# Kernel optimization log

Measured on AMD Instinct MI355X. Metric: run time of the kernel, lower is better.

The kernel has to match this reference:

```python
import jax, jax.numpy as jnp
import numpy as np

D_MODEL = 1024
N_HEADS = 16
D_HEAD = D_MODEL // N_HEADS
B, T = 4, 2048


def setup_inputs() -> dict:
    key = jax.random.key(0)
    ks = jax.random.split(key, 9)
    s = 0.02
    return {
        "x": jax.random.normal(ks[0], (B, T, D_MODEL), dtype=jnp.float32),
        "Wq": jax.random.normal(ks[1], (D_MODEL, D_MODEL), dtype=jnp.float32) * s,
        "bq": jnp.zeros((D_MODEL,), dtype=jnp.float32),
        "Wk": jax.random.normal(ks[2], (D_MODEL, D_MODEL), dtype=jnp.float32) * s,
        "bk": jnp.zeros((D_MODEL,), dtype=jnp.float32),
        "Wv": jax.random.normal(ks[3], (D_MODEL, D_MODEL), dtype=jnp.float32) * s,
        "bv": jnp.zeros((D_MODEL,), dtype=jnp.float32),
        "Wo": jax.random.normal(ks[4], (D_MODEL, D_MODEL), dtype=jnp.float32) * s,
        "bo": jnp.zeros((D_MODEL,), dtype=jnp.float32),
    }


def reference(x, Wq, bq, Wk, bk, Wv, bv, Wo, bo):
    # Dropout in eval mode (identity), as standard for a correctness baseline.
    Bx, Tx, _ = x.shape
    # torch nn.Linear: y = x @ W.T + b
    Q = x @ Wq.T + bq
    K = x @ Wk.T + bk
    V = x @ Wv.T + bv
    # [B, T, H, Dh] -> [B, H, T, Dh]
    Q = Q.reshape(Bx, Tx, N_HEADS, D_HEAD).transpose(0, 2, 1, 3)
    K = K.reshape(Bx, Tx, N_HEADS, D_HEAD).transpose(0, 2, 1, 3)
    V = V.reshape(Bx, Tx, N_HEADS, D_HEAD).transpose(0, 2, 1, 3)
    scale = 1.0 / jnp.sqrt(jnp.float32(D_HEAD))
    scores = jnp.einsum("bhqd,bhkd->bhqk", Q, K) * scale  # [B,H,T,T]
    # additive causal mask: -1e6 above the diagonal (matches torch.triu trick)
    mask = jnp.triu(jnp.full((Tx, Tx), -1000000.0, dtype=scores.dtype), k=1)
    scores = scores + mask
    attn = jax.nn.softmax(scores, axis=-1)
    out = jnp.einsum("bhqk,bhkd->bhqd", attn, V)  # [B,H,T,Dh]
    out = out.transpose(0, 2, 1, 3).reshape(Bx, Tx, D_MODEL)
    out = out @ Wo.T + bo
    return out
```

## Files before the change

kernel.cpp:

```cpp
#include <hip/hip_runtime.h>
#include <stdint.h>

#define DM 1024
#define HEADS 16
#define DH 64
#define BQ 4
#define TT 2048
#define MTOT (BQ*TT)
#define NQT (TT/64)

typedef __attribute__((ext_vector_type(8))) __bf16 bf16x8;
typedef __attribute__((ext_vector_type(4))) float f32x4;
typedef __attribute__((ext_vector_type(4))) uint32_t u32x4;
typedef unsigned short u16;
typedef __attribute__((ext_vector_type(8))) unsigned short u16x8;

__device__ __forceinline__ u16 f2b(float f) {
  uint32_t u = __builtin_bit_cast(uint32_t, f);
  u = (u + 0x7fffu + ((u >> 16) & 1u)) >> 16;
  return (u16)u;
}

__device__ __forceinline__ uint32_t cvtpk(float lo, float hi) {
  uint32_t r;
  asm("v_cvt_pk_bf16_f32 %0, %1, %2" : "=v"(r) : "v"(lo), "v"(hi));
  return r;
}

__device__ __forceinline__ void gload_lds16(const u16* g, u16* l) {
  __builtin_amdgcn_global_load_lds(
      (const __attribute__((address_space(1))) void*)g,
      (__attribute__((address_space(3))) void*)l, 16, 0, 0);
}

#define NX (MTOT * DM / 4)
#define NW (DM * DM / 4)
__global__ __launch_bounds__(256) void cast_all(const float* __restrict__ x,
                                                const float* __restrict__ Wq,
                                                const float* __restrict__ Wk,
                                                const float* __restrict__ Wv,
                                                const float* __restrict__ Wo,
                                                u16* __restrict__ xb,
                                                u16* __restrict__ wqkvb,
                                                u16* __restrict__ wob) {
  int i = blockIdx.x * 256 + threadIdx.x;
  const float* src; u16* dst;
  if (i < NX)               { src = x;  dst = xb; }
  else if (i < NX + NW)     { src = Wq; dst = wqkvb;          i -= NX; }
  else if (i < NX + 2 * NW) { src = Wk; dst = wqkvb + 4 * NW; i -= NX + NW; }
  else if (i < NX + 3 * NW) { src = Wv; dst = wqkvb + 8 * NW; i -= NX + 2 * NW; }
  else                      { src = Wo; dst = wob;            i -= NX + 3 * NW; }
  float4 v = ((const float4*)src)[i];
  ushort4 o;
  o.x = f2b(v.x); o.y = f2b(v.y); o.z = f2b(v.z); o.w = f2b(v.w);
  ((ushort4*)dst)[i] = o;
}

#define BKq 32
#define NKq (DM / BKq)
#define SLOT_A (256 * BKq)
#define SLOT_E (2 * SLOT_A)

__global__ __launch_bounds__(512, 2) void gemm_qkv8(const u16* __restrict__ A,
                                                    const u16* __restrict__ W,
                                                    const float* __restrict__ bq,
                                                    const float* __restrict__ bk,
                                                    const float* __restrict__ bv,
                                                    u16* __restrict__ Qo,
                                                    u16* __restrict__ Ko,
                                                    u16* __restrict__ Vto,
                                                    float qs) {
  __shared__ u16 lds[4 * SLOT_E];
  const int tid = threadIdx.x, lane = tid & 63, wave = tid >> 6;
  const int fr = lane & 15, g = lane >> 4;
  const int wm = wave >> 2, wn = wave & 3;

  int bid = blockIdx.x;
  bid = (bid & 7) * 48 + (bid >> 3);
  const int bx = bid % 12, by = bid / 12;
  const int m0 = by * 256, n0 = bx * 256;

  const int srow = tid >> 2;
  const int schunk = (tid & 3) ^ ((tid >> 3) & 3);
  const u16* gA0 = A + (size_t)(m0 + srow) * DM + schunk * 8;
  const u16* gA1 = gA0 + (size_t)128 * DM;
  const u16* gB0 = W + (size_t)(n0 + srow) * DM + schunk * 8;
  const u16* gB1 = gB0 + (size_t)128 * DM;
  const int dA0 = wave * 512;
  const int dA1 = 4096 + wave * 512;
  const int dB0 = SLOT_A + wave * 512;
  const int dB1 = SLOT_A + 4096 + wave * 512;

#define STAGE_Ah(slot, kt) {                                 \
    u16* ls = &lds[(slot) * SLOT_E];                         \
    const int ke = (kt) * BKq;                               \
    gload_lds16(gA0 + ke, ls + dA0);                         \
    gload_lds16(gA1 + ke, ls + dA1); }
#define STAGE_Bh(slot, kt) {                                 \
    u16* ls = &lds[(slot) * SLOT_E];                         \
    const int ke = (kt) * BKq;                               \
    gload_lds16(gB0 + ke, ls + dB0);                         \
    gload_lds16(gB1 + ke, ls + dB1); }

  const int rchunk = (g ^ ((fr >> 1) & 3)) * 8;
  const int offA = (wm * 128 + fr) * 32 + rchunk;
  const int offB = SLOT_A + (wn * 64 + fr) * 32 + rchunk;

  f32x4 acc[8][4];
#pragma unroll
  for (int mi = 0; mi < 8; ++mi)
#pragma unroll
    for (int ni = 0; ni < 4; ++ni) acc[mi][ni] = (f32x4){0.f, 0.f, 0.f, 0.f};

  bf16x8 afA[8], bfA[4], afB[8], bfB[4];

#define READ_P1(AFv, BFv, kt) {                              \
    const u16* sl = &lds[((kt) & 3) * SLOT_E];               \
    _Pragma("unroll")                                        \
    for (int mi = 0; mi < 4; ++mi)                           \
      AFv[mi] = *(const bf16x8*)&sl[offA + mi * 512];        \
    _Pragma("unroll")                                        \
    for (int ni = 0; ni < 4; ++ni)                           \
      BFv[ni] = *(const bf16x8*)&sl[offB + ni * 512]; }
#define READ_P2(AFv, kt) {                                   \
    const u16* sl = &lds[((kt) & 3) * SLOT_E];               \
    _Pragma("unroll")                                        \
    for (int mi = 4; mi < 8; ++mi)                           \
      AFv[mi] = *(const bf16x8*)&sl[offA + mi * 512]; }

#define MFMA_P1(AFv, BFv) {                                  \
    __builtin_amdgcn_s_setprio(1);                           \
    _Pragma("unroll")                                        \
    for (int mi = 0; mi < 4; ++mi)                           \
      _Pragma("unroll")                                      \
      for (int ni = 0; ni < 4; ++ni)                         \
        acc[mi][ni] = __builtin_amdgcn_mfma_f32_16x16x32_bf16(AFv[mi], BFv[ni], acc[mi][ni], 0, 0, 0); \
    __builtin_amdgcn_s_setprio(0); }
#define MFMA_P2(AFv, BFv) {                                  \
    __builtin_amdgcn_s_setprio(1);                           \
    _Pragma("unroll")                                        \
    for (int mi = 4; mi < 8; ++mi)                           \
      _Pragma("unroll")                                      \
      for (int ni = 0; ni < 4; ++ni)                         \
        acc[mi][ni] = __builtin_amdgcn_mfma_f32_16x16x32_bf16(AFv[mi], BFv[ni], acc[mi][ni], 0, 0, 0); \
    __builtin_amdgcn_s_setprio(0); }

#define BARQ asm volatile("s_barrier" ::: "memory");
#define WAIT4 asm volatile("s_waitcnt vmcnt(4)" ::: "memory"); BARQ
#define WAIT0 asm volatile("s_waitcnt vmcnt(0)" ::: "memory"); BARQ

#define STEP(AFc, BFc, AFn, BFn, kt, DO_STAGE) {             \
    WAIT4                                                    \
    READ_P1(AFn, BFn, (kt) + 1)                              \
    MFMA_P1(AFc, BFc)                                        \
    if (DO_STAGE) STAGE_Ah(((kt) + 3) & 3, (kt) + 3)         \
    BARQ                                                     \
    READ_P2(AFn, (kt) + 1)                                   \
    MFMA_P2(AFc, BFc)                                        \
    if (DO_STAGE) STAGE_Bh(((kt) + 3) & 3, (kt) + 3) }

  STAGE_Ah(0, 0) STAGE_Bh(0, 0)
  STAGE_Ah(1, 1) STAGE_Bh(1, 1)
  STAGE_Ah(2, 2) STAGE_Bh(2, 2)
  asm volatile("s_waitcnt vmcnt(8)" ::: "memory");
  asm volatile("s_barrier" ::: "memory");
  READ_P1(afA, bfA, 0)
  READ_P2(afA, 0)

  for (int kt = 0; kt < NKq - 4; kt += 2) {
    STEP(afA, bfA, afB, bfB, kt, true)
    STEP(afB, bfB, afA, bfA, kt + 1, true)
  }
  STEP(afA, bfA, afB, bfB, NKq - 4, true)
  STEP(afB, bfB, afA, bfA, NKq - 3, false)
  WAIT0
  READ_P1(afB, bfB, NKq - 1)
  MFMA_P1(afA, bfA)
  BARQ
  READ_P2(afB, NKq - 1)
  MFMA_P2(afA, bfA)
  MFMA_P1(afB, bfB)
  MFMA_P2(afB, bfB)

  const int g4 = g * 4;
  const int seg = n0 >> 10;
  const int nbase = (n0 & 1023) + wn * 64 + fr;
  if (seg == 0) {
#pragma unroll
    for (int ni = 0; ni < 4; ++ni) {
      const int cgl = nbase + ni * 16;
      const float bb = bq[cgl];
      const int hh = cgl >> 6, d = cgl & 63;
#pragma unroll
      for (int mi = 0; mi < 8; ++mi) {
        const int m = m0 + wm * 128 + mi * 16 + g4;
        const int bi = m >> 11, t = m & 2047;
        u16* dst = &Qo[(((size_t)bi * HEADS + hh) * TT + t) * DH + d];
#pragma unroll
        for (int j = 0; j < 4; ++j)
          dst[(size_t)j * DH] = f2b((acc[mi][ni][j] + bb) * qs);
      }
    }
  } else if (seg == 1) {
#pragma unroll
    for (int ni = 0; ni < 4; ++ni) {
      const int cgl = nbase + ni * 16;
      const float bb = bk[cgl];
      const int hh = cgl >> 6, d = cgl & 63;
#pragma unroll
      for (int mi = 0; mi < 8; ++mi) {
        const int m = m0 + wm * 128 + mi * 16 + g4;
        const int bi = m >> 11, t = m & 2047;
        u16* dst = &Ko[(((size_t)bi * HEADS + hh) * TT + t) * DH + d];
#pragma unroll
        for (int j = 0; j < 4; ++j)
          dst[(size_t)j * DH] = f2b(acc[mi][ni][j] + bb);
      }
    }
  } else {
#pragma unroll
    for (int ni = 0; ni < 4; ++ni) {
      const int cgl = nbase + ni * 16;
      const float bb = bv[cgl];
      const int hh = cgl >> 6, d = cgl & 63;
#pragma unroll
      for (int mi = 0; mi < 8; ++mi) {
        const int t0 = (m0 + wm * 128 + mi * 16 + g4) & 2047;
        const int bi = (m0 + wm * 128 + mi * 16 + g4) >> 11;
        const int w64 = t0 & 63;
        const int pos = (t0 & ~63) | (((w64 >> 5) & 1) << 5) | (((w64 >> 2) & 3) << 3) |
                        (((w64 >> 4) & 1) << 2);
        ushort4 o;
        o.x = f2b(acc[mi][ni][0] + bb);
        o.y = f2b(acc[mi][ni][1] + bb);
        o.z = f2b(acc[mi][ni][2] + bb);
        o.w = f2b(acc[mi][ni][3] + bb);
        *(ushort4*)&Vto[(((size_t)bi * HEADS + hh) * DH + d) * TT + pos] = o;
      }
    }
  }
#undef STAGE_Ah
#undef STAGE_Bh
#undef READ_P1
#undef READ_P2
#undef MFMA_P1
#undef MFMA_P2
#undef STEP
#undef BARQ
#undef WAIT4
#undef WAIT0
}

#define SLOT_OA (256 * 32)
#define SLOT_OB (128 * 32)
#define SLOT_OE (SLOT_OA + SLOT_OB)

__global__ __launch_bounds__(512, 2) void gemm_out8(const u16* __restrict__ A,
                                                    const u16* __restrict__ Bw,
                                                    const float* __restrict__ bias,
                                                    float* __restrict__ outp) {
  __shared__ u16 lds[4 * SLOT_OE];
  const int tid = threadIdx.x, lane = tid & 63, wave = tid >> 6;
  const int fr = lane & 15, g = lane >> 4;
  const int wm = wave >> 1, wn = wave & 1;

  const int bx = blockIdx.x >> 5, by = blockIdx.x & 31;
  const int m0 = by * 256, n0 = bx * 128;

  const int srow = tid >> 2;
  const int schunk = (tid & 3) ^ ((tid >> 3) & 3);
  const u16* gA0 = A + (size_t)(m0 + srow) * DM + schunk * 8;
  const u16* gA1 = gA0 + (size_t)128 * DM;
  const u16* gB0 = Bw + (size_t)(n0 + srow) * DM + schunk * 8;
  const int dA0 = wave * 512;
  const int dA1 = 4096 + wave * 512;
  const int dB0 = SLOT_OA + wave * 512;

#define STAGEO(slot, kt) {                                   \
    u16* ls = &lds[(slot) * SLOT_OE];                        \
    const int ke = (kt) * 32;                                \
    gload_lds16(gA0 + ke, ls + dA0);                         \
    gload_lds16(gA1 + ke, ls + dA1);                         \
    gload_lds16(gB0 + ke, ls + dB0); }

  const int rchunk = (g ^ ((fr >> 1) & 3)) * 8;
  const int offA = (wm * 64 + fr) * 32 + rchunk;
  const int offB = SLOT_OA + (wn * 64 + fr) * 32 + rchunk;

  f32x4 acc[4][4];
#pragma unroll
  for (int mi = 0; mi < 4; ++mi)
#pragma unroll
    for (int ni = 0; ni < 4; ++ni) acc[mi][ni] = (f32x4){0.f, 0.f, 0.f, 0.f};

  bf16x8 afA[4], bfA[4], afB[4], bfB[4];

#define READO(AFv, BFv, kt) {                                \
    const u16* sl = &lds[((kt) & 3) * SLOT_OE];              \
    _Pragma("unroll")                                        \
    for (int mi = 0; mi < 4; ++mi)                           \
      AFv[mi] = *(const bf16x8*)&sl[offA + mi * 512];        \
    _Pragma("unroll")                                        \
    for (int ni = 0; ni < 4; ++ni)                           \
      BFv[ni] = *(const bf16x8*)&sl[offB + ni * 512]; }

#define MFMAO(AFv, BFv) {                                    \
    __builtin_amdgcn_s_setprio(1);                           \
    _Pragma("unroll")                                        \
    for (int mi = 0; mi < 4; ++mi)                           \
      _Pragma("unroll")                                      \
      for (int ni = 0; ni < 4; ++ni)                         \
        acc[mi][ni] = __builtin_amdgcn_mfma_f32_16x16x32_bf16(AFv[mi], BFv[ni], acc[mi][ni], 0, 0, 0); \
    __builtin_amdgcn_s_setprio(0); }

#define OW3 asm volatile("s_waitcnt vmcnt(3)" ::: "memory"); \
            asm volatile("s_barrier" ::: "memory");
#define OW0 asm volatile("s_waitcnt vmcnt(0)" ::: "memory"); \
            asm volatile("s_barrier" ::: "memory");

  STAGEO(0, 0)
  STAGEO(1, 1)
  STAGEO(2, 2)
  asm volatile("s_waitcnt vmcnt(6)" ::: "memory");
  asm volatile("s_barrier" ::: "memory");
  READO(afA, bfA, 0)

  for (int kt = 0; kt < 28; kt += 2) {
    OW3
    READO(afB, bfB, kt + 1)
    MFMAO(afA, bfA)
    STAGEO((kt + 3) & 3, kt + 3)
    OW3
    READO(afA, bfA, kt + 2)
    MFMAO(afB, bfB)
    STAGEO((kt + 4) & 3, kt + 4)
  }
  OW3
  READO(afB, bfB, 29)
  MFMAO(afA, bfA)
  STAGEO(3, 31)
  OW3
  READO(afA, bfA, 30)
  MFMAO(afB, bfB)
  OW0
  READO(afB, bfB, 31)
  MFMAO(afA, bfA)
  MFMAO(afB, bfB)

  const int g4 = g * 4;
#pragma unroll
  for (int mi = 0; mi < 4; ++mi) {
    const int rg = m0 + wm * 64 + mi * 16 + g4;
#pragma unroll
    for (int ni = 0; ni < 4; ++ni) {
      const int cg = n0 + wn * 64 + ni * 16 + fr;
      const float bb = bias[cg];
#pragma unroll
      for (int j = 0; j < 4; ++j)
        outp[(size_t)(rg + j) * DM + cg] = acc[mi][ni][j] + bb;
    }
  }
#undef STAGEO
#undef READO
#undef MFMAO
#undef OW3
#undef OW0
}

__global__ __launch_bounds__(256) void attn_fwd(const u16* __restrict__ Q,
                                                const u16* __restrict__ K,
                                                const u16* __restrict__ Vt,
                                                u16* __restrict__ O) {
  const int o_ = blockIdx.x;
  const int xcd = o_ & 7, j = o_ >> 3;
  const int gi = j & 7;
  const int qt = 31 - (j >> 3);
  const int gidx = xcd * 8 + gi;
  const int b = gidx >> 4, h = gidx & 15;
  const int tid = threadIdx.x, lane = tid & 63, wave = tid >> 6;
  __shared__ u16 Ks[64 * 64];
  __shared__ u16 Vs[64 * 64];

  const size_t bh = ((size_t)b * HEADS + h) * TT;
  const size_t vbse = ((size_t)b * HEADS + h) * DH;
  const int fr = lane & 15, g = lane >> 4;
  const int sr = tid >> 2;
  const int sc0 = tid & 3;

  const int sw1 = (sc0 ^ (sr & 7)) * 8;
  const int sw2 = ((sc0 + 4) ^ (sr & 7)) * 8;
  const int sgc = sc0 * 8;
  const int rk0 = (g ^ (fr & 7)) * 8;
  const int rk1 = ((4 + g) ^ (fr & 7)) * 8;
  const int k8 = g * 8;

  const int q0 = qt * 64;
  const int qrow = q0 + wave * 16 + fr;
  const bf16x8 qf0 = *(const bf16x8*)&Q[(bh + qrow) * DH + k8];
  const bf16x8 qf1 = *(const bf16x8*)&Q[(bh + qrow) * DH + 32 + k8];

  float lsum = 0.f;
  f32x4 oacc[4];
#pragma unroll
  for (int c = 0; c < 4; ++c) oacc[c] = (f32x4){0.f, 0.f, 0.f, 0.f};

  for (int kvb = 0; kvb <= qt; ++kvb) {
    const int kv0 = kvb * 64;
    {
      const u16* kg = &K[(bh + kv0 + sr) * DH + sgc];
      u16x8 ka = *(const u16x8*)kg;
      u16x8 kc = *(const u16x8*)(kg + 32);
      const u16* vg = &Vt[(vbse + sr) * TT + kv0 + sgc];
      u16x8 va = *(const u16x8*)vg;
      u16x8 vc = *(const u16x8*)(vg + 32);
      *(u16x8*)&Ks[sr * 64 + sw1] = ka;
      *(u16x8*)&Ks[sr * 64 + sw2] = kc;
      *(u16x8*)&Vs[sr * 64 + sw1] = va;
      *(u16x8*)&Vs[sr * 64 + sw2] = vc;
    }
    __syncthreads();

    f32x4 s[4];
    __builtin_amdgcn_s_setprio(1);
#pragma unroll
    for (int c = 0; c < 4; ++c) {
      bf16x8 kb0 = *(const bf16x8*)&Ks[(c * 16 + fr) * 64 + rk0];
      bf16x8 kb1 = *(const bf16x8*)&Ks[(c * 16 + fr) * 64 + rk1];
      f32x4 t = (f32x4){0.f, 0.f, 0.f, 0.f};
      t = __builtin_amdgcn_mfma_f32_16x16x32_bf16(kb0, qf0, t, 0, 0, 0);
      t = __builtin_amdgcn_mfma_f32_16x16x32_bf16(kb1, qf1, t, 0, 0, 0);
      s[c] = t;
    }
    __builtin_amdgcn_s_setprio(0);

    if (kvb == qt) {
#pragma unroll
      for (int c = 0; c < 4; ++c) {
        const int colg = kv0 + c * 16 + 4 * g;
#pragma unroll
        for (int r = 0; r < 4; ++r)
          if (colg + r > qrow) s[c][r] = -1e30f;
      }
    }

    float rs = 0.f;
    uint32_t pk[8];
#pragma unroll
    for (int c = 0; c < 4; ++c) {
      float p0 = __builtin_amdgcn_exp2f(s[c][0]);
      float p1 = __builtin_amdgcn_exp2f(s[c][1]);
      float p2 = __builtin_amdgcn_exp2f(s[c][2]);
      float p3 = __builtin_amdgcn_exp2f(s[c][3]);
      rs += (p0 + p1) + (p2 + p3);
      pk[2 * c] = cvtpk(p0, p1);
      pk[2 * c + 1] = cvtpk(p2, p3);
    }
    rs += __shfl_xor(rs, 16);
    rs += __shfl_xor(rs, 32);
    lsum += rs;

    const bf16x8 pa0 = __builtin_bit_cast(bf16x8, (u32x4){pk[0], pk[1], pk[2], pk[3]});
    const bf16x8 pa1 = __builtin_bit_cast(bf16x8, (u32x4){pk[4], pk[5], pk[6], pk[7]});

    __builtin_amdgcn_s_setprio(1);
#pragma unroll
    for (int c = 0; c < 4; ++c) {
      bf16x8 vb0 = *(const bf16x8*)&Vs[(c * 16 + fr) * 64 + rk0];
      bf16x8 vb1 = *(const bf16x8*)&Vs[(c * 16 + fr) * 64 + rk1];
      oacc[c] = __builtin_amdgcn_mfma_f32_16x16x32_bf16(vb0, pa0, oacc[c], 0, 0, 0);
      oacc[c] = __builtin_amdgcn_mfma_f32_16x16x32_bf16(vb1, pa1, oacc[c], 0, 0, 0);
    }
    __builtin_amdgcn_s_setprio(0);
    __syncthreads();
  }

  const float inv = 1.f / lsum;
#pragma unroll
  for (int c = 0; c < 4; ++c) {
    ushort4 o;
    o.x = f2b(oacc[c][0] * inv);
    o.y = f2b(oacc[c][1] * inv);
    o.z = f2b(oacc[c][2] * inv);
    o.w = f2b(oacc[c][3] * inv);
    *(ushort4*)&O[((size_t)b * TT + qrow) * DM + h * DH + c * 16 + 4 * g] = o;
  }
}

extern "C" void kernel_launch(void* const* d_in, const int* in_sizes, int n_in,
                              void* d_out, int out_size, void* d_ws, size_t ws_size,
                              hipStream_t stream) {
  const float* x  = (const float*)d_in[0];
  const float* Wq = (const float*)d_in[1];
  const float* bq = (const float*)d_in[2];
  const float* Wk = (const float*)d_in[3];
  const float* bk = (const float*)d_in[4];
  const float* Wv = (const float*)d_in[5];
  const float* bv = (const float*)d_in[6];
  const float* Wo = (const float*)d_in[7];
  const float* bo = (const float*)d_in[8];

  char* w = (char*)d_ws;
  u16* xb    = (u16*)w; w += (size_t)MTOT * DM * 2;
  u16* Wqkvb = (u16*)w; w += (size_t)3 * DM * DM * 2;
  u16* Wob   = (u16*)w; w += (size_t)DM * DM * 2;
  u16* Qb    = (u16*)w; w += (size_t)MTOT * DM * 2;
  u16* Kb    = (u16*)w; w += (size_t)MTOT * DM * 2;
  u16* Vtb   = (u16*)w; w += (size_t)MTOT * DM * 2;
  u16* AOb   = (u16*)w; w += (size_t)MTOT * DM * 2;

  cast_all<<<(NX + 4 * NW) / 256, 256, 0, stream>>>(x, Wq, Wk, Wv, Wo, xb, Wqkvb, Wob);

  const float qs = 0.125f * 1.44269504f;
  gemm_qkv8<<<384, 512, 0, stream>>>(xb, Wqkvb, bq, bk, bv, Qb, Kb, Vtb, qs);

  attn_fwd<<<2048, 256, 0, stream>>>(Qb, Kb, Vtb, AOb);

  gemm_out8<<<256, 512, 0, stream>>>(AOb, Wob, bo, (float*)d_out);
}
```

Before: 160.0 us.

## Shrink QKV GEMM tile to 256x128 and process two query tiles per attention block

The QKV projection GEMM moves from 256x256 to 256x128 output tiles with a simplified single-phase pipeline, doubling the grid from 384 to 768 blocks for better CU coverage. The attention kernel now handles 128 query rows per block (two 64-row halves sharing each K/V tile load from LDS), halving the block count and the K/V traffic per query. The trade-offs are lower arithmetic intensity in the GEMM, more registers per attention thread, and coarser causal load balancing with extra wasted masked work in the last tiles.

```diff
diff --git a/kernel.cpp b/kernel.cpp
--- a/kernel.cpp
+++ b/kernel.cpp
@@ -56,10 +56,9 @@
   ((ushort4*)dst)[i] = o;
 }
 
-#define BKq 32
-#define NKq (DM / BKq)
-#define SLOT_A (256 * BKq)
-#define SLOT_E (2 * SLOT_A)
+#define SLOT_QA (256 * 32)
+#define SLOT_QB (128 * 32)
+#define SLOT_QE (SLOT_QA + SLOT_QB)
 
 __global__ __launch_bounds__(512, 2) void gemm_qkv8(const u16* __restrict__ A,
                                                     const u16* __restrict__ W,
@@ -70,65 +69,54 @@
                                                     u16* __restrict__ Ko,
                                                     u16* __restrict__ Vto,
                                                     float qs) {
-  __shared__ u16 lds[4 * SLOT_E];
+  __shared__ u16 lds[4 * SLOT_QE];
   const int tid = threadIdx.x, lane = tid & 63, wave = tid >> 6;
   const int fr = lane & 15, g = lane >> 4;
-  const int wm = wave >> 2, wn = wave & 3;
+  const int wm = wave >> 1, wn = wave & 1;
 
   int bid = blockIdx.x;
-  bid = (bid & 7) * 48 + (bid >> 3);
-  const int bx = bid % 12, by = bid / 12;
-  const int m0 = by * 256, n0 = bx * 256;
+  bid = (bid & 7) * 96 + (bid >> 3);
+  const int by = bid / 24, bx = bid % 24;
+  const int m0 = by * 256, n0 = bx * 128;
 
   const int srow = tid >> 2;
   const int schunk = (tid & 3) ^ ((tid >> 3) & 3);
   const u16* gA0 = A + (size_t)(m0 + srow) * DM + schunk * 8;
   const u16* gA1 = gA0 + (size_t)128 * DM;
   const u16* gB0 = W + (size_t)(n0 + srow) * DM + schunk * 8;
-  const u16* gB1 = gB0 + (size_t)128 * DM;
   const int dA0 = wave * 512;
   const int dA1 = 4096 + wave * 512;
-  const int dB0 = SLOT_A + wave * 512;
-  const int dB1 = SLOT_A + 4096 + wave * 512;
-
-#define STAGE_Ah(slot, kt) {                                 \
-    u16* ls = &lds[(slot) * SLOT_E];                         \
-    const int ke = (kt) * BKq;                               \
+  const int dB0 = SLOT_QA + wave * 512;
+
+#define STAGEQ(slot, kt) {                                   \
+    u16* ls = &lds[(slot) * SLOT_QE];                        \
+    const int ke = (kt) * 32;                                \
     gload_lds16(gA0 + ke, ls + dA0);                         \
-    gload_lds16(gA1 + ke, ls + dA1); }
-#define STAGE_Bh(slot, kt) {                                 \
-    u16* ls = &lds[(slot) * SLOT_E];                         \
-    const int ke = (kt) * BKq;                               \
-    gload_lds16(gB0 + ke, ls + dB0);                         \
-    gload_lds16(gB1 + ke, ls + dB1); }
+    gload_lds16(gA1 + ke, ls + dA1);                         \
+    gload_lds16(gB0 + ke, ls + dB0); }
 
   const int rchunk = (g ^ ((fr >> 1) & 3)) * 8;
-  const int offA = (wm * 128 + fr) * 32 + rchunk;
-  const int offB = SLOT_A + (wn * 64 + fr) * 32 + rchunk;
-
-  f32x4 acc[8][4];
-#pragma unroll
-  for (int mi = 0; mi < 8; ++mi)
+  const int offA = (wm * 64 + fr) * 32 + rchunk;
+  const int offB = SLOT_QA + (wn * 64 + fr) * 32 + rchunk;
+
+  f32x4 acc[4][4];
+#pragma unroll
+  for (int mi = 0; mi < 4; ++mi)
 #pragma unroll
     for (int ni = 0; ni < 4; ++ni) acc[mi][ni] = (f32x4){0.f, 0.f, 0.f, 0.f};
 
-  bf16x8 afA[8], bfA[4], afB[8], bfB[4];
-
-#define READ_P1(AFv, BFv, kt) {                              \
-    const u16* sl = &lds[((kt) & 3) * SLOT_E];               \
+  bf16x8 afA[4], bfA[4], afB[4], bfB[4];
+
+#define READQ(AFv, BFv, kt) {                                \
+    const u16* sl = &lds[((kt) & 3) * SLOT_QE];              \
     _Pragma("unroll")                                        \
     for (int mi = 0; mi < 4; ++mi)                           \
       AFv[mi] = *(const bf16x8*)&sl[offA + mi * 512];        \
     _Pragma("unroll")                                        \
     for (int ni = 0; ni < 4; ++ni)                           \
       BFv[ni] = *(const bf16x8*)&sl[offB + ni * 512]; }
-#define READ_P2(AFv, kt) {                                   \
-    const u16* sl = &lds[((kt) & 3) * SLOT_E];               \
-    _Pragma("unroll")                                        \
-    for (int mi = 4; mi < 8; ++mi)                           \
-      AFv[mi] = *(const bf16x8*)&sl[offA + mi * 512]; }
-
-#define MFMA_P1(AFv, BFv) {                                  \
+
+#define MFMAQ(AFv, BFv) {                                    \
     __builtin_amdgcn_s_setprio(1);                           \
     _Pragma("unroll")                                        \
     for (int mi = 0; mi < 4; ++mi)                           \
@@ -136,51 +124,40 @@
       for (int ni = 0; ni < 4; ++ni)                         \
         acc[mi][ni] = __builtin_amdgcn_mfma_f32_16x16x32_bf16(AFv[mi], BFv[ni], acc[mi][ni], 0, 0, 0); \
     __builtin_amdgcn_s_setprio(0); }
-#define MFMA_P2(AFv, BFv) {                                  \
-    __builtin_amdgcn_s_setprio(1);                           \
-    _Pragma("unroll")                                        \
-    for (int mi = 4; mi < 8; ++mi)                           \
-      _Pragma("unroll")                                      \
-      for (int ni = 0; ni < 4; ++ni)                         \
-        acc[mi][ni] = __builtin_amdgcn_mfma_f32_16x16x32_bf16(AFv[mi], BFv[ni], acc[mi][ni], 0, 0, 0); \
-    __builtin_amdgcn_s_setprio(0); }
-
-#define BARQ asm volatile("s_barrier" ::: "memory");
-#define WAIT4 asm volatile("s_waitcnt vmcnt(4)" ::: "memory"); BARQ
-#define WAIT0 asm volatile("s_waitcnt vmcnt(0)" ::: "memory"); BARQ
-
-#define STEP(AFc, BFc, AFn, BFn, kt, DO_STAGE) {             \
-    WAIT4                                                    \
-    READ_P1(AFn, BFn, (kt) + 1)                              \
-    MFMA_P1(AFc, BFc)                                        \
-    if (DO_STAGE) STAGE_Ah(((kt) + 3) & 3, (kt) + 3)         \
-    BARQ                                                     \
-    READ_P2(AFn, (kt) + 1)                                   \
-    MFMA_P2(AFc, BFc)                                        \
-    if (DO_STAGE) STAGE_Bh(((kt) + 3) & 3, (kt) + 3) }
-
-  STAGE_Ah(0, 0) STAGE_Bh(0, 0)
-  STAGE_Ah(1, 1) STAGE_Bh(1, 1)
-  STAGE_Ah(2, 2) STAGE_Bh(2, 2)
-  asm volatile("s_waitcnt vmcnt(8)" ::: "memory");
+
+#define QW3 asm volatile("s_waitcnt vmcnt(3)" ::: "memory"); \
+            asm volatile("s_barrier" ::: "memory");
+#define QW0 asm volatile("s_waitcnt vmcnt(0)" ::: "memory"); \
+            asm volatile("s_barrier" ::: "memory");
+
+  STAGEQ(0, 0)
+  STAGEQ(1, 1)
+  STAGEQ(2, 2)
+  asm volatile("s_waitcnt vmcnt(6)" ::: "memory");
   asm volatile("s_barrier" ::: "memory");
-  READ_P1(afA, bfA, 0)
-  READ_P2(afA, 0)
-
-  for (int kt = 0; kt < NKq - 4; kt += 2) {
-    STEP(afA, bfA, afB, bfB, kt, true)
-    STEP(afB, bfB, afA, bfA, kt + 1, true)
-  }
-  STEP(afA, bfA, afB, bfB, NKq - 4, true)
-  STEP(afB, bfB, afA, bfA, NKq - 3, false)
-  WAIT0
-  READ_P1(afB, bfB, NKq - 1)
-  MFMA_P1(afA, bfA)
-  BARQ
-  READ_P2(afB, NKq - 1)
-  MFMA_P2(afA, bfA)
-  MFMA_P1(afB, bfB)
-  MFMA_P2(afB, bfB)
+  READQ(afA, bfA, 0)
+
+  for (int kt = 0; kt < 28; kt += 2) {
+    QW3
+    READQ(afB, bfB, kt + 1)
+    MFMAQ(afA, bfA)
+    STAGEQ((kt + 3) & 3, kt + 3)
+    QW3
+    READQ(afA, bfA, kt + 2)
+    MFMAQ(afB, bfB)
+    STAGEQ((kt + 4) & 3, kt + 4)
+  }
+  QW3
+  READQ(afB, bfB, 29)
+  MFMAQ(afA, bfA)
+  STAGEQ(3, 31)
+  QW3
+  READQ(afA, bfA, 30)
+  MFMAQ(afB, bfB)
+  QW0
+  READQ(afB, bfB, 31)
+  MFMAQ(afA, bfA)
+  MFMAQ(afB, bfB)
 
   const int g4 = g * 4;
   const int seg = n0 >> 10;
@@ -192,8 +169,8 @@
       const float bb = bq[cgl];
       const int hh = cgl >> 6, d = cgl & 63;
 #pragma unroll
-      for (int mi = 0; mi < 8; ++mi) {
-        const int m = m0 + wm * 128 + mi * 16 + g4;
+      for (int mi = 0; mi < 4; ++mi) {
+        const int m = m0 + wm * 64 + mi * 16 + g4;
         const int bi = m >> 11, t = m & 2047;
         u16* dst = &Qo[(((size_t)bi * HEADS + hh) * TT + t) * DH + d];
 #pragma unroll
@@ -208,8 +185,8 @@
       const float bb = bk[cgl];
       const int hh = cgl >> 6, d = cgl & 63;
 #pragma unroll
-      for (int mi = 0; mi < 8; ++mi) {
-        const int m = m0 + wm * 128 + mi * 16 + g4;
+      for (int mi = 0; mi < 4; ++mi) {
+        const int m = m0 + wm * 64 + mi * 16 + g4;
         const int bi = m >> 11, t = m & 2047;
         u16* dst = &Ko[(((size_t)bi * HEADS + hh) * TT + t) * DH + d];
 #pragma unroll
@@ -224,9 +201,9 @@
       const float bb = bv[cgl];
       const int hh = cgl >> 6, d = cgl & 63;
 #pragma unroll
-      for (int mi = 0; mi < 8; ++mi) {
-        const int t0 = (m0 + wm * 128 + mi * 16 + g4) & 2047;
-        const int bi = (m0 + wm * 128 + mi * 16 + g4) >> 11;
+      for (int mi = 0; mi < 4; ++mi) {
+        const int m = m0 + wm * 64 + mi * 16 + g4;
+        const int t0 = m & 2047, bi = m >> 11;
         const int w64 = t0 & 63;
         const int pos = (t0 & ~63) | (((w64 >> 5) & 1) << 5) | (((w64 >> 2) & 3) << 3) |
                         (((w64 >> 4) & 1) << 2);
@@ -239,16 +216,11 @@
       }
     }
   }
-#undef STAGE_Ah
-#undef STAGE_Bh
-#undef READ_P1
-#undef READ_P2
-#undef MFMA_P1
-#undef MFMA_P2
-#undef STEP
-#undef BARQ
-#undef WAIT4
-#undef WAIT0
+#undef STAGEQ
+#undef READQ
+#undef MFMAQ
+#undef QW3
+#undef QW0
 }
 
 #define SLOT_OA (256 * 32)
@@ -374,7 +346,7 @@
   const int o_ = blockIdx.x;
   const int xcd = o_ & 7, j = o_ >> 3;
   const int gi = j & 7;
-  const int qt = 31 - (j >> 3);
+  const int qt128 = 15 - (j >> 3);
   const int gidx = xcd * 8 + gi;
   const int b = gidx >> 4, h = gidx & 15;
   const int tid = threadIdx.x, lane = tid & 63, wave = tid >> 6;
@@ -394,17 +366,24 @@
   const int rk1 = ((4 + g) ^ (fr & 7)) * 8;
   const int k8 = g * 8;
 
-  const int q0 = qt * 64;
-  const int qrow = q0 + wave * 16 + fr;
-  const bf16x8 qf0 = *(const bf16x8*)&Q[(bh + qrow) * DH + k8];
-  const bf16x8 qf1 = *(const bf16x8*)&Q[(bh + qrow) * DH + 32 + k8];
-
-  float lsum = 0.f;
-  f32x4 oacc[4];
-#pragma unroll
-  for (int c = 0; c < 4; ++c) oacc[c] = (f32x4){0.f, 0.f, 0.f, 0.f};
-
-  for (int kvb = 0; kvb <= qt; ++kvb) {
+  const int q0 = qt128 * 128;
+  const int qtL = 2 * qt128, qtH = qtL + 1;
+  const int qrowL = q0 + wave * 16 + fr;
+  const int qrowH = q0 + 64 + wave * 16 + fr;
+  const bf16x8 qfL0 = *(const bf16x8*)&Q[(bh + qrowL) * DH + k8];
+  const bf16x8 qfL1 = *(const bf16x8*)&Q[(bh + qrowL) * DH + 32 + k8];
+  const bf16x8 qfH0 = *(const bf16x8*)&Q[(bh + qrowH) * DH + k8];
+  const bf16x8 qfH1 = *(const bf16x8*)&Q[(bh + qrowH) * DH + 32 + k8];
+
+  float lsumL = 0.f, lsumH = 0.f;
+  f32x4 oaccL[4], oaccH[4];
+#pragma unroll
+  for (int c = 0; c < 4; ++c) {
+    oaccL[c] = (f32x4){0.f, 0.f, 0.f, 0.f};
+    oaccH[c] = (f32x4){0.f, 0.f, 0.f, 0.f};
+  }
+
+  for (int kvb = 0; kvb <= qtH; ++kvb) {
     const int kv0 = kvb * 64;
     {
       const u16* kg = &K[(bh + kv0 + sr) * DH + sgc];
@@ -420,69 +399,99 @@
     }
     __syncthreads();
 
-    f32x4 s[4];
+    f32x4 sL[4], sH[4];
     __builtin_amdgcn_s_setprio(1);
 #pragma unroll
     for (int c = 0; c < 4; ++c) {
       bf16x8 kb0 = *(const bf16x8*)&Ks[(c * 16 + fr) * 64 + rk0];
       bf16x8 kb1 = *(const bf16x8*)&Ks[(c * 16 + fr) * 64 + rk1];
-      f32x4 t = (f32x4){0.f, 0.f, 0.f, 0.f};
-      t = __builtin_amdgcn_mfma_f32_16x16x32_bf16(kb0, qf0, t, 0, 0, 0);
-      t = __builtin_amdgcn_mfma_f32_16x16x32_bf16(kb1, qf1, t, 0, 0, 0);
-      s[c] = t;
+      f32x4 tL = (f32x4){0.f, 0.f, 0.f, 0.f};
+      tL = __builtin_amdgcn_mfma_f32_16x16x32_bf16(kb0, qfL0, tL, 0, 0, 0);
+      tL = __builtin_amdgcn_mfma_f32_16x16x32_bf16(kb1, qfL1, tL, 0, 0, 0);
+      sL[c] = tL;
+      f32x4 tH = (f32x4){0.f, 0.f, 0.f, 0.f};
+      tH = __builtin_amdgcn_mfma_f32_16x16x32_bf16(kb0, qfH0, tH, 0, 0, 0);
+      tH = __builtin_amdgcn_mfma_f32_16x16x32_bf16(kb1, qfH1, tH, 0, 0, 0);
+      sH[c] = tH;
     }
     __builtin_amdgcn_s_setprio(0);
 
-    if (kvb == qt) {
+    if (kvb >= qtL) {
 #pragma unroll
       for (int c = 0; c < 4; ++c) {
         const int colg = kv0 + c * 16 + 4 * g;
 #pragma unroll
-        for (int r = 0; r < 4; ++r)
-          if (colg + r > qrow) s[c][r] = -1e30f;
+        for (int r = 0; r < 4; ++r) {
+          if (colg + r > qrowL) sL[c][r] = -1e30f;
+          if (colg + r > qrowH) sH[c][r] = -1e30f;
+        }
       }
     }
 
-    float rs = 0.f;
-    uint32_t pk[8];
+    float rsL = 0.f, rsH = 0.f;
+    uint32_t pkL[8], pkH[8];
 #pragma unroll
     for (int c = 0; c < 4; ++c) {
-      float p0 = __builtin_amdgcn_exp2f(s[c][0]);
-      float p1 = __builtin_amdgcn_exp2f(s[c][1]);
-      float p2 = __builtin_amdgcn_exp2f(s[c][2]);
-      float p3 = __builtin_amdgcn_exp2f(s[c][3]);
-      rs += (p0 + p1) + (p2 + p3);
-      pk[2 * c] = cvtpk(p0, p1);
-      pk[2 * c + 1] = cvtpk(p2, p3);
-    }
-    rs += __shfl_xor(rs, 16);
-    rs += __shfl_xor(rs, 32);
-    lsum += rs;
-
-    const bf16x8 pa0 = __builtin_bit_cast(bf16x8, (u32x4){pk[0], pk[1], pk[2], pk[3]});
-    const bf16x8 pa1 = __builtin_bit_cast(bf16x8, (u32x4){pk[4], pk[5], pk[6], pk[7]});
+      float l0 = __builtin_amdgcn_exp2f(sL[c][0]);
+      float l1 = __builtin_amdgcn_exp2f(sL[c][1]);
+      float l2 = __builtin_amdgcn_exp2f(sL[c][2]);
+      float l3 = __builtin_amdgcn_exp2f(sL[c][3]);
+      rsL += (l0 + l1) + (l2 + l3);
+      pkL[2 * c] = cvtpk(l0, l1);
+      pkL[2 * c + 1] = cvtpk(l2, l3);
+      float h0 = __builtin_amdgcn_exp2f(sH[c][0]);
+      float h1 = __builtin_amdgcn_exp2f(sH[c][1]);
+      float h2 = __builtin_amdgcn_exp2f(sH[c][2]);
+      float h3 = __builtin_amdgcn_exp2f(sH[c][3]);
+      rsH += (h0 + h1) + (h2 + h3);
+      pkH[2 * c] = cvtpk(h0, h1);
+      pkH[2 * c + 1] = cvtpk(h2, h3);
+    }
+    rsL += __shfl_xor(rsL, 16);
+    rsL += __shfl_xor(rsL, 32);
+    lsumL += rsL;
+    rsH += __shfl_xor(rsH, 16);
+    rsH += __shfl_xor(rsH, 32);
+    lsumH += rsH;
+
+    const bf16x8 paL0 = __builtin_bit_cast(bf16x8, (u32x4){pkL[0], pkL[1], pkL[2], pkL[3]});
+    const bf16x8 paL1 = __builtin_bit_cast(bf16x8, (u32x4){pkL[4], pkL[5], pkL[6], pkL[7]});
+    const bf16x8 paH0 = __builtin_bit_cast(bf16x8, (u32x4){pkH[0], pkH[1], pkH[2], pkH[3]});
+    const bf16x8 paH1 = __builtin_bit_cast(bf16x8, (u32x4){pkH[4], pkH[5], pkH[6], pkH[7]});
 
     __builtin_amdgcn_s_setprio(1);
 #pragma unroll
     for (int c = 0; c < 4; ++c) {
       bf16x8 vb0 = *(const bf16x8*)&Vs[(c * 16 + fr) * 64 + rk0];
       bf16x8 vb1 = *(const bf16x8*)&Vs[(c * 16 + fr) * 64 + rk1];
-      oacc[c] = __builtin_amdgcn_mfma_f32_16x16x32_bf16(vb0, pa0, oacc[c], 0, 0, 0);
-      oacc[c] = __builtin_amdgcn_mfma_f32_16x16x32_bf16(vb1, pa1, oacc[c], 0, 0, 0);
+      oaccL[c] = __builtin_amdgcn_mfma_f32_16x16x32_bf16(vb0, paL0, oaccL[c], 0, 0, 0);
+      oaccL[c] = __builtin_amdgcn_mfma_f32_16x16x32_bf16(vb1, paL1, oaccL[c], 0, 0, 0);
+      oaccH[c] = __builtin_amdgcn_mfma_f32_16x16x32_bf16(vb0, paH0, oaccH[c], 0, 0, 0);
+      oaccH[c] = __builtin_amdgcn_mfma_f32_16x16x32_bf16(vb1, paH1, oaccH[c], 0, 0, 0);
     }
     __builtin_amdgcn_s_setprio(0);
     __syncthreads();
   }
 
-  const float inv = 1.f / lsum;
+  const float invL = 1.f / lsumL;
 #pragma unroll
   for (int c = 0; c < 4; ++c) {
     ushort4 o;
-    o.x = f2b(oacc[c][0] * inv);
-    o.y = f2b(oacc[c][1] * inv);
-    o.z = f2b(oacc[c][2] * inv);
-    o.w = f2b(oacc[c][3] * inv);
-    *(ushort4*)&O[((size_t)b * TT + qrow) * DM + h * DH + c * 16 + 4 * g] = o;
+    o.x = f2b(oaccL[c][0] * invL);
+    o.y = f2b(oaccL[c][1] * invL);
+    o.z = f2b(oaccL[c][2] * invL);
+    o.w = f2b(oaccL[c][3] * invL);
+    *(ushort4*)&O[((size_t)b * TT + qrowL) * DM + h * DH + c * 16 + 4 * g] = o;
+  }
+  const float invH = 1.f / lsumH;
+#pragma unroll
+  for (int c = 0; c < 4; ++c) {
+    ushort4 o;
+    o.x = f2b(oaccH[c][0] * invH);
+    o.y = f2b(oaccH[c][1] * invH);
+    o.z = f2b(oaccH[c][2] * invH);
+    o.w = f2b(oaccH[c][3] * invH);
+    *(ushort4*)&O[((size_t)b * TT + qrowH) * DM + h * DH + c * 16 + 4 * g] = o;
   }
 }
 
@@ -511,9 +520,9 @@
   cast_all<<<(NX + 4 * NW) / 256, 256, 0, stream>>>(x, Wq, Wk, Wv, Wo, xb, Wqkvb, Wob);
 
   const float qs = 0.125f * 1.44269504f;
-  gemm_qkv8<<<384, 512, 0, stream>>>(xb, Wqkvb, bq, bk, bv, Qb, Kb, Vtb, qs);
-
-  attn_fwd<<<2048, 256, 0, stream>>>(Qb, Kb, Vtb, AOb);
+  gemm_qkv8<<<768, 512, 0, stream>>>(xb, Wqkvb, bq, bk, bv, Qb, Kb, Vtb, qs);
+
+  attn_fwd<<<1024, 256, 0, stream>>>(Qb, Kb, Vtb, AOb);
 
   gemm_out8<<<256, 512, 0, stream>>>(AOb, Wob, bo, (float*)d_out);
 }
```

New measurement: 155.5 us. 1.03x faster.
